# Kernel optimization log

Hardware: AMD Instinct MI355X
Metric: run time of the kernel (lower is better)

## Reference

```python
import jax, jax.numpy as jnp
import numpy as np

H, D = 16, 64  # num_heads, head_dim (hidden = H*D = 1024)
EPS = 1e-6

def elu_plus_one(x):
    return jax.nn.elu(x) + 1.0

def setup_inputs() -> dict:
    key = jax.random.key(0)
    ks = jax.random.split(key, 12)
    hid = H * D
    s = 0.02
    return {
        "hidden_states": jax.random.normal(ks[0], (1, 2048, hid), jnp.float32),
        "w_q": jax.random.normal(ks[1], (hid, hid), jnp.float32) * s,
        "w_k": jax.random.normal(ks[2], (hid, hid), jnp.float32) * s,
        "w_v": jax.random.normal(ks[3], (hid, hid), jnp.float32) * s,
        "w_o": jax.random.normal(ks[4], (hid, hid), jnp.float32) * s,
        "memory_gate": jnp.zeros((H,), jnp.float32),
        "eg_w1": jax.random.normal(ks[5], (hid, hid // 4), jnp.float32) * s,
        "eg_b1": jnp.zeros((hid // 4,), jnp.float32),
        "eg_w2": jax.random.normal(ks[6], (hid // 4, 1), jnp.float32) * s,
        "eg_b2": jnp.zeros((1,), jnp.float32),
        "fine_mem": jax.random.normal(ks[7], (4, H, D, D), jnp.float32) * s,
        "fine_norm": jax.random.uniform(ks[8], (4, H, D), jnp.float32),
    }

def _retrieve(sigma_q, memory, memory_norm):
    # sigma_q: [b,h,s,d], memory: [h,d,e], memory_norm: [h,d]
    a = jnp.einsum('bhsd,hde->bhse', sigma_q, memory)
    relevance = jnp.einsum('bhsd,hd->bhs', sigma_q, memory_norm)
    out = a / jnp.clip(relevance, EPS, None)[..., None]
    return out, relevance

def reference(hidden_states, w_q, w_k, w_v, w_o, memory_gate,
              eg_w1, eg_b1, eg_w2, eg_b2, fine_mem, fine_norm):
    B, S, hid = hidden_states.shape
    def proj(w):
        return (hidden_states @ w).reshape(B, S, H, D).transpose(0, 2, 1, 3)  # [b,h,s,d]
    q, k, v = proj(w_q), proj(w_k), proj(w_v)
    sigma_q = elu_plus_one(q)

    # coarse memory = sum of fine memories
    M_coarse = fine_mem.sum(0)        # [h,d,d]
    z_coarse = fine_norm.sum(0)       # [h,d]
    output_coarse, _ = _retrieve(sigma_q, M_coarse, z_coarse)  # [b,h,s,d]

    # learned expansion gate on coarse representation
    coarse_repr = output_coarse.transpose(0, 2, 1, 3).reshape(B, S, hid)
    logit = jax.nn.relu(coarse_repr @ eg_w1 + eg_b1) @ eg_w2 + eg_b2  # [b,s,1]
    expansion_prob = jax.nn.sigmoid(logit)                            # [b,s,1]

    # fine-grained retrieval: attention-weighted mix over the 4 banks
    outs = jnp.einsum('bhsd,fhde->fbhse', sigma_q, fine_mem)   # [f,b,h,s,d]
    rels = jnp.einsum('bhsd,fhd->fbhs', sigma_q, fine_norm)    # [f,b,h,s]
    outs = outs / jnp.clip(rels, EPS, None)[..., None]
    weights = jax.nn.softmax(rels.mean(-1), axis=0)            # [f,b,h]
    output_fine = (outs * weights[:, :, :, None, None]).sum(0)  # [b,h,s,d]

    ep = expansion_prob.transpose(0, 2, 1)[..., None]          # [b,1,s,1]
    memory_output = ep * output_fine + (1.0 - ep) * output_coarse

    # causal linear attention within current segment
    sigma_k = elu_plus_one(k)
    kv = jnp.einsum('bhsd,bhse->bhsde', sigma_k, v)            # [b,h,s,d,d]
    kv_cumsum = jnp.cumsum(kv, axis=2)
    k_cumsum = jnp.cumsum(sigma_k, axis=2)
    num = jnp.einsum('bhsd,bhsde->bhse', sigma_q, kv_cumsum)
    den = jnp.clip(jnp.einsum('bhsd,bhsd->bhs', sigma_q, k_cumsum), EPS, None)[..., None]
    local_output = num / den

    gate = jax.nn.sigmoid(memory_gate).reshape(1, H, 1, 1)
    output = gate * memory_output + (1.0 - gate) * local_output
    output = output.transpose(0, 2, 1, 3).reshape(B, S, hid)
    return output @ w_o
```

## Files before the change

### kernel.cpp

```cpp
#include <hip/hip_runtime.h>
#include <cmath>

#define EPSF 1e-6f
#define LDK 72


typedef __attribute__((ext_vector_type(8))) short bf16x8;
typedef __attribute__((ext_vector_type(4))) float f32x4;
typedef __attribute__((ext_vector_type(8))) unsigned short u16x8;

__device__ __forceinline__ float wave_allsum(float v) {
#pragma unroll
  for (int off = 32; off > 0; off >>= 1) v += __shfl_xor(v, off, 64);
  return v;
}

__device__ __forceinline__ unsigned short f2bf(float f) {
  unsigned int u = __float_as_uint(f);
  unsigned int r = (u + 0x7fffu + ((u >> 16) & 1u)) >> 16;
  return (unsigned short)r;
}
__device__ __forceinline__ float bf2f(unsigned short u) {
  return __uint_as_float(((unsigned int)u) << 16);
}

__global__ __launch_bounds__(256) void k0_mcT(const float* __restrict__ FM,
    const float* __restrict__ FN, unsigned short* __restrict__ MCT,
    float* __restrict__ ZC)
{
  int h = blockIdx.x, tid = threadIdx.x;
  __shared__ float tile[64][65];
  for (int i = tid; i < 4096; i += 256) {
    int dp = i >> 6, e = i & 63;
    float s = FM[(0 * 16 + h) * 4096 + i] + FM[(1 * 16 + h) * 4096 + i]
            + FM[(2 * 16 + h) * 4096 + i] + FM[(3 * 16 + h) * 4096 + i];
    tile[dp][e] = s;
  }
  if (tid < 64)
    ZC[h * 64 + tid] = FN[h * 64 + tid] + FN[1024 + h * 64 + tid]
                     + FN[2048 + h * 64 + tid] + FN[3072 + h * 64 + tid];
  __syncthreads();
  for (int i = tid; i < 4096; i += 256) {
    int e = i >> 6, dp = i & 63;
    MCT[h * 4096 + e * 64 + dp] = f2bf(tile[dp][e]);
  }
}

__global__ __launch_bounds__(256) void cast_bf16_k(const float* __restrict__ X,
    unsigned short* __restrict__ Y)
{
  int i = blockIdx.x * 256 + threadIdx.x;
  float4 v = *reinterpret_cast<const float4*>(X + i * 4);
  ushort4 o; o.x = f2bf(v.x); o.y = f2bf(v.y); o.z = f2bf(v.z); o.w = f2bf(v.w);
  *reinterpret_cast<ushort4*>(Y + i * 4) = o;
}

__global__ __launch_bounds__(256) void cast_transpose_k(const float* __restrict__ W,
    unsigned short* __restrict__ WT, int N)
{
  __shared__ float tile[64][65];
  int n0 = blockIdx.x * 64, k0 = blockIdx.y * 64;
  int tid = threadIdx.x;
  for (int i = tid; i < 4096; i += 256) {
    int r = i >> 6, c = i & 63;
    tile[r][c] = W[(k0 + r) * N + n0 + c];
  }
  __syncthreads();
  for (int i = tid; i < 1024; i += 256) {
    int r = i >> 4, c4 = (i & 15) * 4;
    ushort4 o;
    o.x = f2bf(tile[c4 + 0][r]); o.y = f2bf(tile[c4 + 1][r]);
    o.z = f2bf(tile[c4 + 2][r]); o.w = f2bf(tile[c4 + 3][r]);
    *reinterpret_cast<ushort4*>(&WT[(n0 + r) * 1024 + k0 + c4]) = o;
  }
}

__global__ __launch_bounds__(256) void cast_w4(const float* __restrict__ W0,
    const float* __restrict__ W1, const float* __restrict__ W2, const float* __restrict__ W3,
    unsigned short* __restrict__ T0, unsigned short* __restrict__ T1,
    unsigned short* __restrict__ T2, unsigned short* __restrict__ T3)
{
  int z = blockIdx.z;
  const float* W = (z == 0) ? W0 : (z == 1) ? W1 : (z == 2) ? W2 : W3;
  unsigned short* WT = (z == 0) ? T0 : (z == 1) ? T1 : (z == 2) ? T2 : T3;
  __shared__ float tile[64][65];
  int n0 = blockIdx.x * 64, k0 = blockIdx.y * 64;
  int tid = threadIdx.x;
  for (int i = tid; i < 4096; i += 256) {
    int r = i >> 6, c = i & 63;
    tile[r][c] = W[(k0 + r) * 1024 + n0 + c];
  }
  __syncthreads();
  for (int i = tid; i < 1024; i += 256) {
    int r = i >> 4, c4 = (i & 15) * 4;
    ushort4 o;
    o.x = f2bf(tile[c4 + 0][r]); o.y = f2bf(tile[c4 + 1][r]);
    o.z = f2bf(tile[c4 + 2][r]); o.w = f2bf(tile[c4 + 3][r]);
    *reinterpret_cast<ushort4*>(&WT[(n0 + r) * 1024 + k0 + c4]) = o;
  }
}

__global__ __launch_bounds__(256) void fm_cast_t(const float* __restrict__ FM,
    unsigned short* __restrict__ FMT)
{
  __shared__ float tile[64][65];
  int b = blockIdx.x, tid = threadIdx.x;
  const float* src = FM + b * 4096;
  for (int i = tid; i < 4096; i += 256) tile[i >> 6][i & 63] = src[i];
  __syncthreads();
  unsigned short* dst = FMT + b * 4096;
  for (int i = tid; i < 4096; i += 256) {
    int e = i >> 6, dp = i & 63;
    dst[e * 64 + dp] = f2bf(tile[dp][e]);
  }
}

__global__ __launch_bounds__(256) void mm_bf16(const unsigned short* __restrict__ A,
    const unsigned short* __restrict__ BT, float* __restrict__ C, int ldc, int act)
{
  __shared__ unsigned short As[128 * LDK];
  __shared__ unsigned short Bs[128 * LDK];
  int tid = threadIdx.x;
  int m0 = blockIdx.y * 128, n0 = blockIdx.x * 128;
  int wid = tid >> 6, lane = tid & 63;
  int wr = wid >> 1, wc = wid & 1;
  int lr = lane & 15, lg = lane >> 4;

  f32x4 acc[4][4];
#pragma unroll
  for (int m = 0; m < 4; ++m)
#pragma unroll
    for (int n = 0; n < 4; ++n)
#pragma unroll
      for (int r = 0; r < 4; ++r) acc[m][n][r] = 0.f;

  for (int kt = 0; kt < 16; ++kt) {
    int k0 = kt * 64;
#pragma unroll
    for (int p = 0; p < 4; ++p) {
      int c = p * 256 + tid;
      int row = c >> 3, k8 = c & 7;
      u16x8 va = *reinterpret_cast<const u16x8*>(A + (m0 + row) * 1024 + k0 + k8 * 8);
      *reinterpret_cast<u16x8*>(&As[row * LDK + k8 * 8]) = va;
      u16x8 vb = *reinterpret_cast<const u16x8*>(BT + (n0 + row) * 1024 + k0 + k8 * 8);
      *reinterpret_cast<u16x8*>(&Bs[row * LDK + k8 * 8]) = vb;
    }
    __syncthreads();
#pragma unroll
    for (int kk = 0; kk < 2; ++kk) {
      bf16x8 af[4], bfr[4];
#pragma unroll
      for (int m = 0; m < 4; ++m)
        af[m] = *reinterpret_cast<const bf16x8*>(&As[(wr * 64 + m * 16 + lr) * LDK + kk * 32 + lg * 8]);
#pragma unroll
      for (int n = 0; n < 4; ++n)
        bfr[n] = *reinterpret_cast<const bf16x8*>(&Bs[(wc * 64 + n * 16 + lr) * LDK + kk * 32 + lg * 8]);
#pragma unroll
      for (int m = 0; m < 4; ++m)
#pragma unroll
        for (int n = 0; n < 4; ++n)
          acc[m][n] = __builtin_amdgcn_mfma_f32_16x16x32_bf16(af[m], bfr[n], acc[m][n], 0, 0, 0);
    }
    __syncthreads();
  }
#pragma unroll
  for (int m = 0; m < 4; ++m)
#pragma unroll
    for (int n = 0; n < 4; ++n)
#pragma unroll
      for (int r = 0; r < 4; ++r) {
        float v = acc[m][n][r];
        if (act) v = v > 0.f ? v + 1.f : expf(v);
        C[(m0 + wr * 64 + m * 16 + lg * 4 + r) * ldc + n0 + wc * 64 + n * 16 + lr] = v;
      }
}

__global__ __launch_bounds__(256) void proj_bf16(const unsigned short* __restrict__ A,
    const unsigned short* __restrict__ WqT, const unsigned short* __restrict__ WkT,
    const unsigned short* __restrict__ WvT,
    unsigned short* __restrict__ Oq, unsigned short* __restrict__ Ok,
    unsigned short* __restrict__ Ov)
{
  int z = blockIdx.z;
  const unsigned short* BT = (z == 0) ? WqT : (z == 1) ? WkT : WvT;
  unsigned short* C = (z == 0) ? Oq : (z == 1) ? Ok : Ov;

  __shared__ unsigned short As[128 * LDK];
  __shared__ unsigned short Bs[128 * LDK];
  int tid = threadIdx.x;
  int m0 = blockIdx.y * 128, n0 = blockIdx.x * 128;
  int wid = tid >> 6, lane = tid & 63;
  int wr = wid >> 1, wc = wid & 1;
  int lr = lane & 15, lg = lane >> 4;
  int act = (z < 2) ? 1 : 0;

  f32x4 acc[4][4];
#pragma unroll
  for (int m = 0; m < 4; ++m)
#pragma unroll
    for (int n = 0; n < 4; ++n)
#pragma unroll
      for (int r = 0; r < 4; ++r) acc[m][n][r] = 0.f;

  for (int kt = 0; kt < 16; ++kt) {
    int k0 = kt * 64;
#pragma unroll
    for (int p = 0; p < 4; ++p) {
      int c = p * 256 + tid;
      int row = c >> 3, k8 = c & 7;
      u16x8 va = *reinterpret_cast<const u16x8*>(A + (m0 + row) * 1024 + k0 + k8 * 8);
      *reinterpret_cast<u16x8*>(&As[row * LDK + k8 * 8]) = va;
      u16x8 vb = *reinterpret_cast<const u16x8*>(BT + (n0 + row) * 1024 + k0 + k8 * 8);
      *reinterpret_cast<u16x8*>(&Bs[row * LDK + k8 * 8]) = vb;
    }
    __syncthreads();
#pragma unroll
    for (int kk = 0; kk < 2; ++kk) {
      bf16x8 af[4], bfr[4];
#pragma unroll
      for (int m = 0; m < 4; ++m)
        af[m] = *reinterpret_cast<const bf16x8*>(&As[(wr * 64 + m * 16 + lr) * LDK + kk * 32 + lg * 8]);
#pragma unroll
      for (int n = 0; n < 4; ++n)
        bfr[n] = *reinterpret_cast<const bf16x8*>(&Bs[(wc * 64 + n * 16 + lr) * LDK + kk * 32 + lg * 8]);
#pragma unroll
      for (int m = 0; m < 4; ++m)
#pragma unroll
        for (int n = 0; n < 4; ++n)
          acc[m][n] = __builtin_amdgcn_mfma_f32_16x16x32_bf16(af[m], bfr[n], acc[m][n], 0, 0, 0);
    }
    __syncthreads();
  }
#pragma unroll
  for (int m = 0; m < 4; ++m)
#pragma unroll
    for (int n = 0; n < 4; ++n)
#pragma unroll
      for (int r = 0; r < 4; ++r) {
        float v = acc[m][n][r];
        if (act) v = v > 0.f ? v + 1.f : expf(v);
        C[(m0 + wr * 64 + m * 16 + lg * 4 + r) * 1024 + n0 + wc * 64 + n * 16 + lr] = f2bf(v);
      }
}

__global__ __launch_bounds__(256) void eg_fin(const float* __restrict__ H1,
    const float* __restrict__ B1, const float* __restrict__ W2,
    const float* __restrict__ B2, float* __restrict__ EP)
{
  int wid = threadIdx.x >> 6, lane = threadIdx.x & 63;
  int s = blockIdx.x * 4 + wid;
  float4 h = *reinterpret_cast<const float4*>(H1 + s * 256 + lane * 4);
  float4 b = *reinterpret_cast<const float4*>(B1 + lane * 4);
  float4 w = *reinterpret_cast<const float4*>(W2 + lane * 4);
  float v = fmaxf(h.x + b.x, 0.f) * w.x + fmaxf(h.y + b.y, 0.f) * w.y
          + fmaxf(h.z + b.z, 0.f) * w.z + fmaxf(h.w + b.w, 0.f) * w.w;
  v = wave_allsum(v);
  if (lane == 0) EP[s] = 1.f / (1.f + expf(-(v + B2[0])));
}

__global__ __launch_bounds__(256) void rels_kernel(const unsigned short* __restrict__ SQB,
    const float* __restrict__ ZC, const float* __restrict__ FN,
    float* __restrict__ RELC, float* __restrict__ RELS, float* __restrict__ PARTS)
{
  int h = blockIdx.x, st = blockIdx.y, tid = threadIdx.x;
  int s0 = st * 64;
  __shared__ float sqT[64][68];
  __shared__ float zf[5][64];
  __shared__ float relb[5][64];
#pragma unroll
  for (int p = 0; p < 2; ++p) {
    int cidx = p * 256 + tid;
    int r = cidx >> 3, d8 = cidx & 7;
    u16x8 v = *reinterpret_cast<const u16x8*>(SQB + (s0 + r) * 1024 + h * 64 + d8 * 8);
#pragma unroll
    for (int j = 0; j < 8; ++j) sqT[d8 * 8 + j][r] = bf2f((unsigned short)v[j]);
  }
  for (int idx = tid; idx < 320; idx += 256) {
    int w = idx >> 6, d = idx & 63;
    zf[w][d] = (w == 0) ? ZC[h * 64 + d] : FN[(w - 1) * 1024 + h * 64 + d];
  }
  __syncthreads();
  {
    int s = tid & 63, wh = tid >> 6;
    float r = 0.f;
    for (int dp = 0; dp < 64; ++dp) r += sqT[dp][s] * zf[wh][dp];
    relb[wh][s] = r;
    if (wh == 0) {
      float r4 = 0.f;
      for (int dp = 0; dp < 64; ++dp) r4 += sqT[dp][s] * zf[4][dp];
      relb[4][s] = r4;
    }
  }
  __syncthreads();
  if (tid < 64) {
    RELC[h * 2048 + s0 + tid] = relb[0][tid];
#pragma unroll
    for (int f = 0; f < 4; ++f)
      RELS[f * 32768 + h * 2048 + s0 + tid] = relb[1 + f][tid];
#pragma unroll
    for (int f = 0; f < 4; ++f) {
      float v = wave_allsum(relb[1 + f][tid]);
      if (tid == 0) PARTS[f * 512 + h * 32 + st] = v;
    }
  }
}

__global__ __launch_bounds__(256) void coarse_mfma(const unsigned short* __restrict__ SQB,
    const unsigned short* __restrict__ MCT, const float* __restrict__ RELC,
    float* __restrict__ CO, unsigned short* __restrict__ COB)
{
  int h = blockIdx.x, st = blockIdx.y, tid = threadIdx.x;
  int w = tid >> 6, lane = tid & 63, lr = lane & 15, lg = lane >> 4;
  int s0 = st * 128;
  __shared__ unsigned short A_lds[128 * LDK];
  __shared__ unsigned short B_lds[64 * LDK];
#pragma unroll
  for (int p = 0; p < 4; ++p) {
    int c = p * 256 + tid;
    int row = c >> 3, k8 = c & 7;
    *reinterpret_cast<u16x8*>(&A_lds[row * LDK + k8 * 8]) =
        *reinterpret_cast<const u16x8*>(SQB + (s0 + row) * 1024 + h * 64 + k8 * 8);
  }
#pragma unroll
  for (int p = 0; p < 2; ++p) {
    int c = p * 256 + tid;
    int e = c >> 3, k8 = c & 7;
    *reinterpret_cast<u16x8*>(&B_lds[e * LDK + k8 * 8]) =
        *reinterpret_cast<const u16x8*>(MCT + h * 4096 + e * 64 + k8 * 8);
  }
  __syncthreads();

  f32x4 acc[2][4];
#pragma unroll
  for (int m = 0; m < 2; ++m)
#pragma unroll
    for (int n = 0; n < 4; ++n)
#pragma unroll
      for (int r = 0; r < 4; ++r) acc[m][n][r] = 0.f;

#pragma unroll
  for (int kk = 0; kk < 2; ++kk) {
    bf16x8 af[2], bfr[4];
#pragma unroll
    for (int m = 0; m < 2; ++m)
      af[m] = *reinterpret_cast<const bf16x8*>(&A_lds[(w * 32 + m * 16 + lr) * LDK + kk * 32 + lg * 8]);
#pragma unroll
    for (int n = 0; n < 4; ++n)
      bfr[n] = *reinterpret_cast<const bf16x8*>(&B_lds[(n * 16 + lr) * LDK + kk * 32 + lg * 8]);
#pragma unroll
    for (int m = 0; m < 2; ++m)
#pragma unroll
      for (int n = 0; n < 4; ++n)
        acc[m][n] = __builtin_amdgcn_mfma_f32_16x16x32_bf16(af[m], bfr[n], acc[m][n], 0, 0, 0);
  }
#pragma unroll
  for (int m = 0; m < 2; ++m)
#pragma unroll
    for (int r = 0; r < 4; ++r) {
      int s = s0 + w * 32 + m * 16 + lg * 4 + r;
      float rc = fmaxf(RELC[h * 2048 + s], EPSF);
#pragma unroll
      for (int n = 0; n < 4; ++n) {
        float v = acc[m][n][r] / rc;
        CO[s * 1024 + h * 64 + n * 16 + lr] = v;
        COB[s * 1024 + h * 64 + n * 16 + lr] = f2bf(v);
      }
    }
}

__global__ void weights_kernel(const float* __restrict__ P, float* __restrict__ W)
{
  int h = threadIdx.x;
  if (h >= 16) return;
  float r[4];
#pragma unroll
  for (int f = 0; f < 4; ++f) {
    float s = 0.f;
    for (int t = 0; t < 32; ++t) s += P[f * 512 + h * 32 + t];
    r[f] = s * (1.f / 2048.f);
  }
  float m = fmaxf(fmaxf(r[0], r[1]), fmaxf(r[2], r[3]));
  float e0 = expf(r[0] - m), e1 = expf(r[1] - m), e2 = expf(r[2] - m), e3 = expf(r[3] - m);
  float inv = 1.f / (e0 + e1 + e2 + e3);
  W[0 * 16 + h] = e0 * inv; W[1 * 16 + h] = e1 * inv;
  W[2 * 16 + h] = e2 * inv; W[3 * 16 + h] = e3 * inv;
}

__global__ __launch_bounds__(256) void fine_mfma(const unsigned short* __restrict__ SQB,
    const unsigned short* __restrict__ FMT, const float* __restrict__ RELS,
    const float* __restrict__ WT, const float* __restrict__ EP,
    const float* __restrict__ CO, float* __restrict__ MO)
{
  int h = blockIdx.x, st = blockIdx.y;
  int tid = threadIdx.x;
  int w = tid >> 6, lane = tid & 63;
  int lr = lane & 15, lg = lane >> 4;
  int s0 = st * 128;

  __shared__ unsigned short A_lds[128 * LDK];
  __shared__ unsigned short B_lds[4 * 64 * LDK];
  __shared__ float w4s[4];
  if (tid < 4) w4s[tid] = WT[tid * 16 + h];

#pragma unroll
  for (int p = 0; p < 4; ++p) {
    int c = p * 256 + tid;
    int row = c >> 3, k8 = c & 7;
    *reinterpret_cast<u16x8*>(&A_lds[row * LDK + k8 * 8]) =
        *reinterpret_cast<const u16x8*>(SQB + (s0 + row) * 1024 + h * 64 + k8 * 8);
  }
#pragma unroll
  for (int p = 0; p < 8; ++p) {
    int c = p * 256 + tid;
    int f = c >> 9, rem = c & 511;
    int e = rem >> 3, k8 = rem & 7;
    *reinterpret_cast<u16x8*>(&B_lds[(f * 64 + e) * LDK + k8 * 8]) =
        *reinterpret_cast<const u16x8*>(FMT + (f * 16 + h) * 4096 + e * 64 + k8 * 8);
  }
  __syncthreads();

  f32x4 acc[4][2][4];
#pragma unroll
  for (int f = 0; f < 4; ++f)
#pragma unroll
    for (int m = 0; m < 2; ++m)
#pragma unroll
      for (int n = 0; n < 4; ++n)
#pragma unroll
        for (int r = 0; r < 4; ++r) acc[f][m][n][r] = 0.f;

#pragma unroll
  for (int kk = 0; kk < 2; ++kk) {
    bf16x8 af[2];
#pragma unroll
    for (int m = 0; m < 2; ++m)
      af[m] = *reinterpret_cast<const bf16x8*>(&A_lds[(w * 32 + m * 16 + lr) * LDK + kk * 32 + lg * 8]);
#pragma unroll
    for (int f = 0; f < 4; ++f) {
      bf16x8 bf4[4];
#pragma unroll
      for (int n = 0; n < 4; ++n)
        bf4[n] = *reinterpret_cast<const bf16x8*>(&B_lds[(f * 64 + n * 16 + lr) * LDK + kk * 32 + lg * 8]);
#pragma unroll
      for (int m = 0; m < 2; ++m)
#pragma unroll
        for (int n = 0; n < 4; ++n)
          acc[f][m][n] = __builtin_amdgcn_mfma_f32_16x16x32_bf16(af[m], bf4[n], acc[f][m][n], 0, 0, 0);
    }
  }

#pragma unroll
  for (int m = 0; m < 2; ++m)
#pragma unroll
    for (int r = 0; r < 4; ++r) {
      int s = s0 + w * 32 + m * 16 + lg * 4 + r;
      float e = EP[s];
      float i0 = w4s[0] / fmaxf(RELS[0 * 32768 + h * 2048 + s], EPSF);
      float i1 = w4s[1] / fmaxf(RELS[1 * 32768 + h * 2048 + s], EPSF);
      float i2 = w4s[2] / fmaxf(RELS[2 * 32768 + h * 2048 + s], EPSF);
      float i3 = w4s[3] / fmaxf(RELS[3 * 32768 + h * 2048 + s], EPSF);
#pragma unroll
      for (int n = 0; n < 4; ++n) {
        int dg = h * 64 + n * 16 + lr;
        float fine = acc[0][m][n][r] * i0 + acc[1][m][n][r] * i1
                   + acc[2][m][n][r] * i2 + acc[3][m][n][r] * i3;
        float cv = CO[s * 1024 + dg];
        MO[s * 1024 + dg] = e * fine + (1.f - e) * cv;
      }
    }
}

__global__ __launch_bounds__(256) void chunk_mfma(const unsigned short* __restrict__ SKB,
    const unsigned short* __restrict__ VVB, float* __restrict__ ST)
{
  int h = blockIdx.x, c = blockIdx.y, tid = threadIdx.x;
  int w = tid >> 6, lane = tid & 63, lr = lane & 15, lg = lane >> 4;
  int sb = c * 64;
  __shared__ unsigned short A_lds[64 * LDK];
  __shared__ unsigned short B_lds[80 * LDK];
#pragma unroll
  for (int p = 0; p < 2; ++p) {
    int cc = p * 256 + tid;
    int t = cc >> 3, e8 = cc & 7;
    u16x8 kv = *reinterpret_cast<const u16x8*>(SKB + (sb + t) * 1024 + h * 64 + e8 * 8);
    u16x8 vv = *reinterpret_cast<const u16x8*>(VVB + (sb + t) * 1024 + h * 64 + e8 * 8);
#pragma unroll
    for (int j = 0; j < 8; ++j) {
      A_lds[(e8 * 8 + j) * LDK + t] = (unsigned short)kv[j];
      B_lds[(e8 * 8 + j) * LDK + t] = (unsigned short)vv[j];
    }
  }
  if (tid < 64) B_lds[64 * LDK + tid] = 0x3F80;
  for (int i = tid; i < 15 * 64; i += 256) {
    int row = 65 + (i >> 6), col = i & 63;
    B_lds[row * LDK + col] = 0;
  }
  __syncthreads();

  f32x4 acc[5];
#pragma unroll
  for (int n = 0; n < 5; ++n)
#pragma unroll
    for (int r = 0; r < 4; ++r) acc[n][r] = 0.f;
#pragma unroll
  for (int kk = 0; kk < 2; ++kk) {
    bf16x8 af = *reinterpret_cast<const bf16x8*>(&A_lds[(w * 16 + lr) * LDK + kk * 32 + lg * 8]);
#pragma unroll
    for (int n = 0; n < 5; ++n) {
      bf16x8 bfr = *reinterpret_cast<const bf16x8*>(&B_lds[(n * 16 + lr) * LDK + kk * 32 + lg * 8]);
      acc[n] = __builtin_amdgcn_mfma_f32_16x16x32_bf16(af, bfr, acc[n], 0, 0, 0);
    }
  }
  float* base = ST + (h * 32 + c) * 4160;
#pragma unroll
  for (int r = 0; r < 4; ++r) {
    int d = w * 16 + lg * 4 + r;
#pragma unroll
    for (int n = 0; n < 4; ++n)
      base[d * 64 + n * 16 + lr] = acc[n][r];
    if (lr == 0) base[4096 + d] = acc[4][r];
  }
}

__global__ __launch_bounds__(256) void scan_kernel(const float* __restrict__ ST,
    unsigned short* __restrict__ STB)
{
  int gidx = blockIdx.x * 256 + threadIdx.x;
  int h = gidx / 4160, idx = gidx - h * 4160;
  if (h >= 16) return;
  float run = 0.f;
#pragma unroll 4
  for (int c = 0; c < 32; ++c) {
    float t = ST[(h * 32 + c) * 4160 + idx];
    STB[(h * 32 + c) * 4160 + idx] = f2bf(run);
    run += t;
  }
}

__global__ __launch_bounds__(256) void lattn_mfma(const unsigned short* __restrict__ SQB,
    const unsigned short* __restrict__ SKB, const unsigned short* __restrict__ VVB,
    const unsigned short* __restrict__ STB, float* __restrict__ OUT)
{
  int h = blockIdx.x, c = blockIdx.y, tid = threadIdx.x;
  int w = tid >> 6, lane = tid & 63, lr = lane & 15, lg = lane >> 4;
  int sb = c * 64;
  const unsigned short* stb = STB + (h * 32 + c) * 4160;

  __shared__ unsigned short A_lds[64 * LDK];
  __shared__ unsigned short K_lds[64 * LDK];
  __shared__ unsigned short P_lds[80 * LDK];
  __shared__ unsigned short V_lds[80 * LDK];
  __shared__ unsigned short S_lds[64 * LDK];

#pragma unroll
  for (int p = 0; p < 2; ++p) {
    int cc = p * 256 + tid;
    int row = cc >> 3, k8 = cc & 7;
    *reinterpret_cast<u16x8*>(&A_lds[row * LDK + k8 * 8]) =
        *reinterpret_cast<const u16x8*>(SQB + (sb + row) * 1024 + h * 64 + k8 * 8);
    *reinterpret_cast<u16x8*>(&K_lds[row * LDK + k8 * 8]) =
        *reinterpret_cast<const u16x8*>(SKB + (sb + row) * 1024 + h * 64 + k8 * 8);
  }
  for (int i = tid; i < 4096; i += 256) {
    int d = i >> 6, e = i & 63;
    P_lds[e * LDK + d] = stb[i];
  }
#pragma unroll
  for (int p = 0; p < 2; ++p) {
    int cc = p * 256 + tid;
    int t = cc >> 3, e8 = cc & 7;
    u16x8 v = *reinterpret_cast<const u16x8*>(VVB + (sb + t) * 1024 + h * 64 + e8 * 8);
#pragma unroll
    for (int j = 0; j < 8; ++j) V_lds[(e8 * 8 + j) * LDK + t] = (unsigned short)v[j];
  }
  if (tid < 64) {
    P_lds[64 * LDK + tid] = stb[4096 + tid];
    V_lds[64 * LDK + tid] = 0x3F80;
  }
  for (int i = tid; i < 15 * 64; i += 256) {
    int row = 65 + (i >> 6), col = i & 63;
    P_lds[row * LDK + col] = 0;
    V_lds[row * LDK + col] = 0;
  }
  __syncthreads();

  f32x4 acc_i[5];
#pragma unroll
  for (int n = 0; n < 5; ++n)
#pragma unroll
    for (int r = 0; r < 4; ++r) acc_i[n][r] = 0.f;
#pragma unroll
  for (int kk = 0; kk < 2; ++kk) {
    bf16x8 af = *reinterpret_cast<const bf16x8*>(&A_lds[(w * 16 + lr) * LDK + kk * 32 + lg * 8]);
#pragma unroll
    for (int n = 0; n < 5; ++n) {
      bf16x8 bfr = *reinterpret_cast<const bf16x8*>(&P_lds[(n * 16 + lr) * LDK + kk * 32 + lg * 8]);
      acc_i[n] = __builtin_amdgcn_mfma_f32_16x16x32_bf16(af, bfr, acc_i[n], 0, 0, 0);
    }
  }
  f32x4 acc_s[4];
#pragma unroll
  for (int n = 0; n < 4; ++n)
#pragma unroll
    for (int r = 0; r < 4; ++r) acc_s[n][r] = 0.f;
#pragma unroll
  for (int kk = 0; kk < 2; ++kk) {
    bf16x8 af = *reinterpret_cast<const bf16x8*>(&A_lds[(w * 16 + lr) * LDK + kk * 32 + lg * 8]);
#pragma unroll
    for (int n = 0; n < 4; ++n) {
      bf16x8 bfr = *reinterpret_cast<const bf16x8*>(&K_lds[(n * 16 + lr) * LDK + kk * 32 + lg * 8]);
      acc_s[n] = __builtin_amdgcn_mfma_f32_16x16x32_bf16(af, bfr, acc_s[n], 0, 0, 0);
    }
  }
#pragma unroll
  for (int n = 0; n < 4; ++n)
#pragma unroll
    for (int r = 0; r < 4; ++r) {
      int s_loc = w * 16 + lg * 4 + r, t = n * 16 + lr;
      float v = (t <= s_loc) ? acc_s[n][r] : 0.f;
      S_lds[s_loc * LDK + t] = f2bf(v);
    }
  __syncthreads();
  f32x4 acc_p[5];
#pragma unroll
  for (int n = 0; n < 5; ++n)
#pragma unroll
    for (int r = 0; r < 4; ++r) acc_p[n][r] = 0.f;
#pragma unroll
  for (int kk = 0; kk < 2; ++kk) {
    bf16x8 af = *reinterpret_cast<const bf16x8*>(&S_lds[(w * 16 + lr) * LDK + kk * 32 + lg * 8]);
#pragma unroll
    for (int n = 0; n < 5; ++n) {
      bf16x8 bfr = *reinterpret_cast<const bf16x8*>(&V_lds[(n * 16 + lr) * LDK + kk * 32 + lg * 8]);
      acc_p[n] = __builtin_amdgcn_mfma_f32_16x16x32_bf16(af, bfr, acc_p[n], 0, 0, 0);
    }
  }
#pragma unroll
  for (int r = 0; r < 4; ++r) {
    float den = acc_i[4][r] + acc_p[4][r];
    den = __shfl(den, lane & 48);
    den = fmaxf(den, EPSF);
    int s = sb + w * 16 + lg * 4 + r;
#pragma unroll
    for (int n = 0; n < 4; ++n)
      OUT[s * 1024 + h * 64 + n * 16 + lr] = (acc_i[n][r] + acc_p[n][r]) / den;
  }
}

__global__ __launch_bounds__(256) void combine_bf16(const float* __restrict__ MO,
    const float* __restrict__ LO, const float* __restrict__ MG,
    unsigned short* __restrict__ CBB)
{
  int i = blockIdx.x * 256 + threadIdx.x;
  float4 m4 = *reinterpret_cast<const float4*>(MO + i * 4);
  float4 l4 = *reinterpret_cast<const float4*>(LO + i * 4);
  int hh = ((i * 4) >> 6) & 15;
  float g = 1.f / (1.f + expf(-MG[hh]));
  ushort4 o;
  o.x = f2bf(g * m4.x + (1.f - g) * l4.x);
  o.y = f2bf(g * m4.y + (1.f - g) * l4.y);
  o.z = f2bf(g * m4.z + (1.f - g) * l4.z);
  o.w = f2bf(g * m4.w + (1.f - g) * l4.w);
  *reinterpret_cast<ushort4*>(CBB + i * 4) = o;
}

extern "C" void kernel_launch(void* const* d_in, const int* in_sizes, int n_in,
                              void* d_out, int out_size, void* d_ws, size_t ws_size,
                              hipStream_t stream)
{
  const float* hs   = (const float*)d_in[0];
  const float* wq   = (const float*)d_in[1];
  const float* wk   = (const float*)d_in[2];
  const float* wv   = (const float*)d_in[3];
  const float* wo   = (const float*)d_in[4];
  const float* mg   = (const float*)d_in[5];
  const float* egw1 = (const float*)d_in[6];
  const float* egb1 = (const float*)d_in[7];
  const float* egw2 = (const float*)d_in[8];
  const float* egb2 = (const float*)d_in[9];
  const float* fm   = (const float*)d_in[10];
  const float* fn   = (const float*)d_in[11];
  float* out = (float*)d_out;

  float* ws     = (float*)d_ws;
  float* co     = ws;
  float* mo     = co + 2097152;
  float* lo     = mo + 2097152;
  float* zc     = lo + 2097152;
  float* rels   = zc + 1024;
  float* parts  = rels + 131072;
  float* wts    = parts + 2048;
  float* ep     = wts + 64;
  float* relc   = ep + 2048;
  float* states = relc + 32768;
  float* h1     = states + 2129920;
  unsigned short* hsb  = (unsigned short*)(h1 + 524288);
  unsigned short* sqb  = hsb + 2097152;
  unsigned short* skb  = sqb + 2097152;
  unsigned short* vvb  = skb + 2097152;
  unsigned short* cob  = vvb + 2097152;
  unsigned short* cbb  = cob + 2097152;
  unsigned short* wqT  = cbb + 2097152;
  unsigned short* wkT  = wqT + 1048576;
  unsigned short* wvT  = wkT + 1048576;
  unsigned short* woT  = wvT + 1048576;
  unsigned short* w1T  = woT + 1048576;
  unsigned short* fmbT = w1T + 262144;
  unsigned short* mcT  = fmbT + 262144;
  unsigned short* statesb = mcT + 65536;

  k0_mcT<<<16, 256, 0, stream>>>(fm, fn, mcT, zc);
  cast_w4<<<dim3(16, 16, 4), 256, 0, stream>>>(wq, wk, wv, wo, wqT, wkT, wvT, woT);
  cast_transpose_k<<<dim3(4, 16), 256, 0, stream>>>(egw1, w1T, 256);
  fm_cast_t<<<64, 256, 0, stream>>>(fm, fmbT);
  cast_bf16_k<<<2048, 256, 0, stream>>>(hs, hsb);
  proj_bf16<<<dim3(8, 16, 3), 256, 0, stream>>>(hsb, wqT, wkT, wvT, sqb, skb, vvb);
  rels_kernel<<<dim3(16, 32), 256, 0, stream>>>(sqb, zc, fn, relc, rels, parts);
  coarse_mfma<<<dim3(16, 16), 256, 0, stream>>>(sqb, mcT, relc, co, cob);
  mm_bf16<<<dim3(2, 16), 256, 0, stream>>>(cob, w1T, h1, 256, 0);
  eg_fin<<<512, 256, 0, stream>>>(h1, egb1, egw2, egb2, ep);
  weights_kernel<<<1, 64, 0, stream>>>(parts, wts);
  fine_mfma<<<dim3(16, 16), 256, 0, stream>>>(sqb, fmbT, rels, wts, ep, co, mo);
  chunk_mfma<<<dim3(16, 32), 256, 0, stream>>>(skb, vvb, states);
  scan_kernel<<<260, 256, 0, stream>>>(states, statesb);
  lattn_mfma<<<dim3(16, 32), 256, 0, stream>>>(sqb, skb, vvb, statesb, lo);
  combine_bf16<<<2048, 256, 0, stream>>>(mo, lo, mg, cbb);
  mm_bf16<<<dim3(8, 16), 256, 0, stream>>>(cbb, woT, out, 1024, 0);
}
```

Before: 144.3 us.

## Use direct global-to-LDS loads in GEMMs and drop fp32 coarse buffer

Both bf16 GEMM kernels now fill shared memory with global_load_lds (direct global-to-LDS DMA) instead of going through registers, and drop the padded LDS row stride. Separately, the coarse retrieval output is no longer written as fp32; fine_mfma reads the bf16 copy instead. This cuts register traffic and an 8 MB global write/read. The risks are LDS bank conflicts from the unpadded stride and slightly lower precision in the coarse term.

```diff
diff --git a/kernel.cpp b/kernel.cpp
--- a/kernel.cpp
+++ b/kernel.cpp
@@ -3,6 +3,7 @@
 
 #define EPSF 1e-6f
 #define LDK 72
+#define LDG 64
 
 
 typedef __attribute__((ext_vector_type(8))) short bf16x8;
@@ -22,6 +23,12 @@
 }
 __device__ __forceinline__ float bf2f(unsigned short u) {
   return __uint_as_float(((unsigned int)u) << 16);
+}
+
+__device__ __forceinline__ void gload_lds16(const unsigned short* g, unsigned short* l) {
+  __builtin_amdgcn_global_load_lds(
+      (const __attribute__((address_space(1))) unsigned int*)(const void*)g,
+      (__attribute__((address_space(3))) unsigned int*)(void*)l, 16, 0, 0);
 }
 
 __global__ __launch_bounds__(256) void k0_mcT(const float* __restrict__ FM,
@@ -118,13 +125,14 @@
 __global__ __launch_bounds__(256) void mm_bf16(const unsigned short* __restrict__ A,
     const unsigned short* __restrict__ BT, float* __restrict__ C, int ldc, int act)
 {
-  __shared__ unsigned short As[128 * LDK];
-  __shared__ unsigned short Bs[128 * LDK];
+  __shared__ __align__(16) unsigned short As[128 * LDG];
+  __shared__ __align__(16) unsigned short Bs[128 * LDG];
   int tid = threadIdx.x;
   int m0 = blockIdx.y * 128, n0 = blockIdx.x * 128;
   int wid = tid >> 6, lane = tid & 63;
   int wr = wid >> 1, wc = wid & 1;
   int lr = lane & 15, lg = lane >> 4;
+  int srow = lane >> 3, scol = (lane & 7) * 8;
 
   f32x4 acc[4][4];
 #pragma unroll
@@ -138,12 +146,10 @@
     int k0 = kt * 64;
 #pragma unroll
     for (int p = 0; p < 4; ++p) {
-      int c = p * 256 + tid;
-      int row = c >> 3, k8 = c & 7;
-      u16x8 va = *reinterpret_cast<const u16x8*>(A + (m0 + row) * 1024 + k0 + k8 * 8);
-      *reinterpret_cast<u16x8*>(&As[row * LDK + k8 * 8]) = va;
-      u16x8 vb = *reinterpret_cast<const u16x8*>(BT + (n0 + row) * 1024 + k0 + k8 * 8);
-      *reinterpret_cast<u16x8*>(&Bs[row * LDK + k8 * 8]) = vb;
+      int chunk = wid * 4 + p;
+      int row = chunk * 8 + srow;
+      gload_lds16(A  + (m0 + row) * 1024 + k0 + scol, As + chunk * 512);
+      gload_lds16(BT + (n0 + row) * 1024 + k0 + scol, Bs + chunk * 512);
     }
     __syncthreads();
 #pragma unroll
@@ -151,10 +157,10 @@
       bf16x8 af[4], bfr[4];
 #pragma unroll
       for (int m = 0; m < 4; ++m)
-        af[m] = *reinterpret_cast<const bf16x8*>(&As[(wr * 64 + m * 16 + lr) * LDK + kk * 32 + lg * 8]);
+        af[m] = *reinterpret_cast<const bf16x8*>(&As[(wr * 64 + m * 16 + lr) * LDG + kk * 32 + lg * 8]);
 #pragma unroll
       for (int n = 0; n < 4; ++n)
-        bfr[n] = *reinterpret_cast<const bf16x8*>(&Bs[(wc * 64 + n * 16 + lr) * LDK + kk * 32 + lg * 8]);
+        bfr[n] = *reinterpret_cast<const bf16x8*>(&Bs[(wc * 64 + n * 16 + lr) * LDG + kk * 32 + lg * 8]);
 #pragma unroll
       for (int m = 0; m < 4; ++m)
 #pragma unroll
@@ -185,13 +191,14 @@
   const unsigned short* BT = (z == 0) ? WqT : (z == 1) ? WkT : WvT;
   unsigned short* C = (z == 0) ? Oq : (z == 1) ? Ok : Ov;
 
-  __shared__ unsigned short As[128 * LDK];
-  __shared__ unsigned short Bs[128 * LDK];
+  __shared__ __align__(16) unsigned short As[128 * LDG];
+  __shared__ __align__(16) unsigned short Bs[128 * LDG];
   int tid = threadIdx.x;
   int m0 = blockIdx.y * 128, n0 = blockIdx.x * 128;
   int wid = tid >> 6, lane = tid & 63;
   int wr = wid >> 1, wc = wid & 1;
   int lr = lane & 15, lg = lane >> 4;
+  int srow = lane >> 3, scol = (lane & 7) * 8;
   int act = (z < 2) ? 1 : 0;
 
   f32x4 acc[4][4];
@@ -206,12 +213,10 @@
     int k0 = kt * 64;
 #pragma unroll
     for (int p = 0; p < 4; ++p) {
-      int c = p * 256 + tid;
-      int row = c >> 3, k8 = c & 7;
-      u16x8 va = *reinterpret_cast<const u16x8*>(A + (m0 + row) * 1024 + k0 + k8 * 8);
-      *reinterpret_cast<u16x8*>(&As[row * LDK + k8 * 8]) = va;
-      u16x8 vb = *reinterpret_cast<const u16x8*>(BT + (n0 + row) * 1024 + k0 + k8 * 8);
-      *reinterpret_cast<u16x8*>(&Bs[row * LDK + k8 * 8]) = vb;
+      int chunk = wid * 4 + p;
+      int row = chunk * 8 + srow;
+      gload_lds16(A  + (m0 + row) * 1024 + k0 + scol, As + chunk * 512);
+      gload_lds16(BT + (n0 + row) * 1024 + k0 + scol, Bs + chunk * 512);
     }
     __syncthreads();
 #pragma unroll
@@ -219,10 +224,10 @@
       bf16x8 af[4], bfr[4];
 #pragma unroll
       for (int m = 0; m < 4; ++m)
-        af[m] = *reinterpret_cast<const bf16x8*>(&As[(wr * 64 + m * 16 + lr) * LDK + kk * 32 + lg * 8]);
+        af[m] = *reinterpret_cast<const bf16x8*>(&As[(wr * 64 + m * 16 + lr) * LDG + kk * 32 + lg * 8]);
 #pragma unroll
       for (int n = 0; n < 4; ++n)
-        bfr[n] = *reinterpret_cast<const bf16x8*>(&Bs[(wc * 64 + n * 16 + lr) * LDK + kk * 32 + lg * 8]);
+        bfr[n] = *reinterpret_cast<const bf16x8*>(&Bs[(wc * 64 + n * 16 + lr) * LDG + kk * 32 + lg * 8]);
 #pragma unroll
       for (int m = 0; m < 4; ++m)
 #pragma unroll
@@ -307,7 +312,7 @@
 
 __global__ __launch_bounds__(256) void coarse_mfma(const unsigned short* __restrict__ SQB,
     const unsigned short* __restrict__ MCT, const float* __restrict__ RELC,
-    float* __restrict__ CO, unsigned short* __restrict__ COB)
+    unsigned short* __restrict__ COB)
 {
   int h = blockIdx.x, st = blockIdx.y, tid = threadIdx.x;
   int w = tid >> 6, lane = tid & 63, lr = lane & 15, lg = lane >> 4;
@@ -360,11 +365,8 @@
       int s = s0 + w * 32 + m * 16 + lg * 4 + r;
       float rc = fmaxf(RELC[h * 2048 + s], EPSF);
 #pragma unroll
-      for (int n = 0; n < 4; ++n) {
-        float v = acc[m][n][r] / rc;
-        CO[s * 1024 + h * 64 + n * 16 + lr] = v;
-        COB[s * 1024 + h * 64 + n * 16 + lr] = f2bf(v);
-      }
+      for (int n = 0; n < 4; ++n)
+        COB[s * 1024 + h * 64 + n * 16 + lr] = f2bf(acc[m][n][r] / rc);
     }
 }
 
@@ -389,7 +391,7 @@
 __global__ __launch_bounds__(256) void fine_mfma(const unsigned short* __restrict__ SQB,
     const unsigned short* __restrict__ FMT, const float* __restrict__ RELS,
     const float* __restrict__ WT, const float* __restrict__ EP,
-    const float* __restrict__ CO, float* __restrict__ MO)
+    const unsigned short* __restrict__ COB, float* __restrict__ MO)
 {
   int h = blockIdx.x, st = blockIdx.y;
   int tid = threadIdx.x;
@@ -464,7 +466,7 @@
         int dg = h * 64 + n * 16 + lr;
         float fine = acc[0][m][n][r] * i0 + acc[1][m][n][r] * i1
                    + acc[2][m][n][r] * i2 + acc[3][m][n][r] * i3;
-        float cv = CO[s * 1024 + dg];
+        float cv = bf2f(COB[s * 1024 + dg]);
         MO[s * 1024 + dg] = e * fine + (1.f - e) * cv;
       }
     }
@@ -683,8 +685,7 @@
   float* out = (float*)d_out;
 
   float* ws     = (float*)d_ws;
-  float* co     = ws;
-  float* mo     = co + 2097152;
+  float* mo     = ws;
   float* lo     = mo + 2097152;
   float* zc     = lo + 2097152;
   float* rels   = zc + 1024;
@@ -716,11 +717,11 @@
   cast_bf16_k<<<2048, 256, 0, stream>>>(hs, hsb);
   proj_bf16<<<dim3(8, 16, 3), 256, 0, stream>>>(hsb, wqT, wkT, wvT, sqb, skb, vvb);
   rels_kernel<<<dim3(16, 32), 256, 0, stream>>>(sqb, zc, fn, relc, rels, parts);
-  coarse_mfma<<<dim3(16, 16), 256, 0, stream>>>(sqb, mcT, relc, co, cob);
+  coarse_mfma<<<dim3(16, 16), 256, 0, stream>>>(sqb, mcT, relc, cob);
   mm_bf16<<<dim3(2, 16), 256, 0, stream>>>(cob, w1T, h1, 256, 0);
   eg_fin<<<512, 256, 0, stream>>>(h1, egb1, egw2, egb2, ep);
   weights_kernel<<<1, 64, 0, stream>>>(parts, wts);
-  fine_mfma<<<dim3(16, 16), 256, 0, stream>>>(sqb, fmbT, rels, wts, ep, co, mo);
+  fine_mfma<<<dim3(16, 16), 256, 0, stream>>>(sqb, fmbT, rels, wts, ep, cob, mo);
   chunk_mfma<<<dim3(16, 32), 256, 0, stream>>>(skb, vvb, states);
   scan_kernel<<<260, 256, 0, stream>>>(states, statesb);
   lattn_mfma<<<dim3(16, 32), 256, 0, stream>>>(sqb, skb, vvb, statesb, lo);
```

New measurement: 150.2 us. 4.1% more time.
